# Optimization experiments

Hardware: AMD Instinct MI355X
Metric: run time of the kernel (lower is better)

The kernel has to match this reference:

```python
import jax, jax.numpy as jnp
import numpy as np

C_Z = 128
C_H = 128
L = 512
EPS = 1e-5


def _layer_norm(x, w, b):
    mu = jnp.mean(x, axis=-1, keepdims=True)
    var = jnp.mean(jnp.square(x - mu), axis=-1, keepdims=True)
    return (x - mu) * jax.lax.rsqrt(var + EPS) * w + b


def setup_inputs() -> dict:
    key = jax.random.key(0)
    ks = jax.random.split(key, 10)
    s_z = 1.0 / np.sqrt(C_Z)
    s_h = 1.0 / np.sqrt(C_H)
    return {
        "z": jax.random.normal(ks[0], (L, L, C_Z), dtype=jnp.float32),
        "pair_mask": jax.random.randint(ks[1], (L, L), 0, 2, dtype=jnp.int32),
        "ln_in_w": jnp.ones((C_Z,), jnp.float32),
        "ln_in_b": jnp.zeros((C_Z,), jnp.float32),
        "ln_out_w": jnp.ones((C_H,), jnp.float32),
        "ln_out_b": jnp.zeros((C_H,), jnp.float32),
        # weights stored [in, out] so forward is x @ W
        "W_proj_a": jax.random.uniform(ks[2], (C_Z, C_H), jnp.float32, -s_z, s_z),
        "W_gate_a": jax.random.uniform(ks[3], (C_Z, C_H), jnp.float32, -s_z, s_z),
        "W_proj_b": jax.random.uniform(ks[4], (C_Z, C_H), jnp.float32, -s_z, s_z),
        "W_gate_b": jax.random.uniform(ks[5], (C_Z, C_H), jnp.float32, -s_z, s_z),
        "W_gate_out": jax.random.uniform(ks[6], (C_Z, C_Z), jnp.float32, -s_z, s_z),
        "W_proj_out": jax.random.uniform(ks[7], (C_H, C_Z), jnp.float32, -s_h, s_h),
    }


def reference(z, pair_mask, ln_in_w, ln_in_b, ln_out_w, ln_out_b,
              W_proj_a, W_gate_a, W_proj_b, W_gate_b, W_gate_out, W_proj_out):
    mask = pair_mask.astype(z.dtype)[..., None]  # [L, L, 1]
    z_ln = _layer_norm(z, ln_in_w, ln_in_b)      # [L, L, c_z]
    a = jax.nn.sigmoid(z_ln @ W_gate_a) * (z_ln @ W_proj_a) * mask  # [L, L, c_h]
    b = jax.nn.sigmoid(z_ln @ W_gate_b) * (z_ln @ W_proj_b) * mask  # [L, L, c_h]
    m = jnp.einsum('ikc,jkc->ijc', a, b)         # channel-batched matmul
    m_ln = _layer_norm(m, ln_out_w, ln_out_b)
    g = jax.nn.sigmoid(z_ln @ W_gate_out)        # [L, L, c_z]
    dz = g * (m_ln @ W_proj_out)
    return dz * mask
```

## Files before the change

### kernel.cpp

```cpp
#include <hip/hip_runtime.h>
#include <stdint.h>

#define LDIM 512
#define LLTOT 262144
#define EPSV 1e-5f

typedef short bf16x8 __attribute__((ext_vector_type(8)));
typedef float f32x4 __attribute__((ext_vector_type(4)));

__device__ __forceinline__ unsigned short f2bf(float f) {
  union { float f; unsigned u; } v; v.f = f;
  unsigned r = v.u + 0x7FFFu + ((v.u >> 16) & 1u);
  return (unsigned short)(r >> 16);
}
__device__ __forceinline__ float bf2f(unsigned short h) {
  union { unsigned u; float f; } v; v.u = ((unsigned)h) << 16;
  return v.f;
}
__device__ __forceinline__ float sigm(float x) { return 1.0f / (1.0f + __expf(-x)); }


__global__ void k_prep(const float* __restrict__ Wpa, const float* __restrict__ Wga,
                       const float* __restrict__ Wpb, const float* __restrict__ Wgb,
                       const float* __restrict__ Wgo, const float* __restrict__ Wpo,
                       unsigned short* __restrict__ Wt) {
  int t = blockIdx.x * blockDim.x + threadIdx.x;
  int mat = t >> 14;
  int rem = t & 16383;
  int o = rem >> 7;
  int c = rem & 127;
  const float* src;
  switch (mat) {
    case 0: src = Wga; break;
    case 1: src = Wpa; break;
    case 2: src = Wgb; break;
    case 3: src = Wpb; break;
    case 4: src = Wgo; break;
    default: src = Wpo; break;
  }
  Wt[mat * 16384 + o * 128 + c] = f2bf(src[c * 128 + o]);
}

__global__ __launch_bounds__(256) void k_proj(const float* __restrict__ z,
                                              const float* __restrict__ lnw,
                                              const float* __restrict__ lnb,
                                              const unsigned short* __restrict__ Wt,
                                              const int* __restrict__ maskp,
                                              unsigned short* __restrict__ a_f,
                                              unsigned short* __restrict__ b_f,
                                              unsigned short* __restrict__ gout) {
  __shared__ unsigned char zbuf[128 * 272];
  __shared__ float maskf[128];
  const int t = threadIdx.x;
  const int bid = blockIdx.x;
  const long r0 = (long)bid * 128;
  const int w = t >> 6, lane = t & 63;
  const int mn = lane & 15, q4 = lane >> 4;
  const int k0 = (bid & 3) * 128;
  const int i16 = bid >> 6;
  const int irem = (bid >> 2) & 15;

  if (t < 128) maskf[t] = (float)maskp[r0 + t];

  const float lw0 = lnw[2 * lane], lw1 = lnw[2 * lane + 1];
  const float lb0 = lnb[2 * lane], lb1 = lnb[2 * lane + 1];
#pragma unroll 2
  for (int rr = 0; rr < 32; rr += 4) {
    float2 v[4];
#pragma unroll
    for (int i = 0; i < 4; ++i)
      v[i] = ((const float2*)(z + (r0 + w * 32 + rr + i) * 128))[lane];
#pragma unroll
    for (int i = 0; i < 4; ++i) {
      float s = v[i].x + v[i].y, q = v[i].x * v[i].x + v[i].y * v[i].y;
#pragma unroll
      for (int off = 32; off; off >>= 1) { s += __shfl_xor(s, off); q += __shfl_xor(q, off); }
      float mu = s * (1.0f / 128.0f);
      float rs = rsqrtf(q * (1.0f / 128.0f) - mu * mu + EPSV);
      ushort2 o;
      o.x = f2bf((v[i].x - mu) * rs * lw0 + lb0);
      o.y = f2bf((v[i].y - mu) * rs * lw1 + lb1);
      ((ushort2*)&zbuf[(w * 32 + rr + i) * 272])[lane] = o;
    }
  }
  __syncthreads();

#pragma unroll 1
  for (int p = 0; p < 2; ++p) {
    const unsigned short* Wg = Wt + (p * 2) * 16384;
    const unsigned short* Wp = Wt + (p * 2 + 1) * 16384;
    unsigned short* dst = p ? b_f : a_f;
    bf16x8 wg[2][4], wp[2][4];
#pragma unroll
    for (int ntl = 0; ntl < 2; ++ntl)
#pragma unroll
      for (int kk = 0; kk < 4; ++kk) {
        const int o = (w * 2 + ntl) * 16 + mn;
        wg[ntl][kk] = *(const bf16x8*)(Wg + o * 128 + kk * 32 + q4 * 8);
        wp[ntl][kk] = *(const bf16x8*)(Wp + o * 128 + kk * 32 + q4 * 8);
      }
#pragma unroll 1
    for (int rg = 0; rg < 8; ++rg) {
      bf16x8 afr[4];
#pragma unroll
      for (int kk = 0; kk < 4; ++kk)
        afr[kk] = *(const bf16x8*)(&zbuf[(rg * 16 + mn) * 272 + kk * 64 + q4 * 16]);
      f32x4 aG[2] = {{0.f,0.f,0.f,0.f},{0.f,0.f,0.f,0.f}};
      f32x4 aP[2] = {{0.f,0.f,0.f,0.f},{0.f,0.f,0.f,0.f}};
#pragma unroll
      for (int kk = 0; kk < 4; ++kk)
#pragma unroll
        for (int ntl = 0; ntl < 2; ++ntl) {
          aG[ntl] = __builtin_amdgcn_mfma_f32_16x16x32_bf16(afr[kk], wg[ntl][kk], aG[ntl], 0, 0, 0);
          aP[ntl] = __builtin_amdgcn_mfma_f32_16x16x32_bf16(afr[kk], wp[ntl][kk], aP[ntl], 0, 0, 0);
        }
      const int rowb = rg * 16 + q4 * 4;
      const int kpos = k0 + rowb;
      const int kc = kpos >> 5;
      const int cell = (irem * 4 + ((kpos >> 3) & 3)) * 16 + (kpos & 7) * 2;
#pragma unroll
      for (int ntl = 0; ntl < 2; ++ntl) {
        const int c = (w * 2 + ntl) * 16 + mn;
        unsigned short hv[4];
#pragma unroll
        for (int r = 0; r < 4; ++r)
          hv[r] = f2bf(sigm(aG[ntl][r]) * aP[ntl][r] * maskf[rowb + r]);
        uint2 pk;
        pk.x = (unsigned)hv[0] | ((unsigned)hv[1] << 16);
        pk.y = (unsigned)hv[2] | ((unsigned)hv[3] << 16);
        *(uint2*)((char*)dst + (long)c * 524288 + kc * 32768 + i16 * 1024 + cell) = pk;
      }
    }
  }

  {
    const unsigned short* Wgp = Wt + 4 * 16384;
    bf16x8 wg[2][4];
#pragma unroll
    for (int ntl = 0; ntl < 2; ++ntl)
#pragma unroll
      for (int kk = 0; kk < 4; ++kk)
        wg[ntl][kk] = *(const bf16x8*)(Wgp + ((w * 2 + ntl) * 16 + mn) * 128 + kk * 32 + q4 * 8);
#pragma unroll 1
    for (int rg = 0; rg < 8; ++rg) {
      bf16x8 afr[4];
#pragma unroll
      for (int kk = 0; kk < 4; ++kk)
        afr[kk] = *(const bf16x8*)(&zbuf[(rg * 16 + mn) * 272 + kk * 64 + q4 * 16]);
      f32x4 aG[2] = {{0.f,0.f,0.f,0.f},{0.f,0.f,0.f,0.f}};
#pragma unroll
      for (int kk = 0; kk < 4; ++kk)
#pragma unroll
        for (int ntl = 0; ntl < 2; ++ntl)
          aG[ntl] = __builtin_amdgcn_mfma_f32_16x16x32_bf16(afr[kk], wg[ntl][kk], aG[ntl], 0, 0, 0);
      const int rowb = rg * 16 + q4 * 4;
#pragma unroll
      for (int ntl = 0; ntl < 2; ++ntl) {
        const int c = (w * 2 + ntl) * 16 + mn;
#pragma unroll
        for (int r = 0; r < 4; ++r)
          gout[(r0 + rowb + r) * 128 + c] = f2bf(sigm(aG[ntl][r]));
      }
    }
  }
}

__global__ __launch_bounds__(256) void k_einsum(const unsigned short* __restrict__ af_g,
                                                const unsigned short* __restrict__ bf_g,
                                                unsigned short* __restrict__ m_t) {
  __shared__ unsigned char shm[36864];
  const int t = threadIdx.x;
  const int w = t >> 6, lane = t & 63;
  const int bid = blockIdx.x;
  const int xcd = bid & 7;
  const int j = bid >> 3;
  const int ch = xcd * 16 + (j >> 4);
  const int tile = j & 15;
  const int ti = tile >> 2, tj = tile & 3;
  const int wr = w >> 1, wc = w & 1;
  const int mn = lane & 15, q4 = lane >> 4;
  const int loff = (mn * 4 + q4) * 16;
  const char* Af = (const char*)af_g + (long)ch * 524288 + (ti * 8 + wr * 4) * 1024 + loff;
  const char* Bf = (const char*)bf_g + (long)ch * 524288 + (tj * 8 + wc * 4) * 1024 + loff;

  f32x4 acc[4][4];
#pragma unroll
  for (int i = 0; i < 4; ++i)
#pragma unroll
    for (int jj = 0; jj < 4; ++jj) acc[i][jj] = (f32x4){0.f, 0.f, 0.f, 0.f};

  bf16x8 afr[2][4], bfr[2][4];
#define LOADFRAG(buf, k32)                                                    \
  {                                                                           \
    _Pragma("unroll")                                                         \
    for (int mt = 0; mt < 4; ++mt)                                            \
      afr[buf][mt] = *(const bf16x8*)(Af + (k32) * 32768 + mt * 1024);        \
    _Pragma("unroll")                                                         \
    for (int nt = 0; nt < 4; ++nt)                                            \
      bfr[buf][nt] = *(const bf16x8*)(Bf + (k32) * 32768 + nt * 1024);        \
  }
#define MFMABLK(buf)                                                          \
  {                                                                           \
    _Pragma("unroll")                                                         \
    for (int mt = 0; mt < 4; ++mt)                                            \
      _Pragma("unroll")                                                       \
      for (int nt = 0; nt < 4; ++nt)                                          \
        acc[mt][nt] = __builtin_amdgcn_mfma_f32_16x16x32_bf16(                \
            afr[buf][mt], bfr[buf][nt], acc[mt][nt], 0, 0, 0);                \
  }

  LOADFRAG(0, 0)
#pragma unroll 1
  for (int k32 = 0; k32 < 14; k32 += 2) {
    LOADFRAG(1, k32 + 1)
    MFMABLK(0)
    LOADFRAG(0, k32 + 2)
    MFMABLK(1)
  }
  LOADFRAG(1, 15)
  MFMABLK(0)
  MFMABLK(1)
#undef LOADFRAG
#undef MFMABLK

  unsigned char* eb = shm + w * 9216;
#pragma unroll
  for (int mt = 0; mt < 4; ++mt)
#pragma unroll
    for (int nt = 0; nt < 4; ++nt)
#pragma unroll
      for (int r = 0; r < 4; ++r) {
        int rl = mt * 16 + q4 * 4 + r;
        int cl = nt * 16 + mn;
        *(unsigned short*)(&eb[rl * 144 + cl * 2]) = f2bf(acc[mt][nt][r]);
      }
  char* Mg = (char*)m_t + (long)ch * 524288 +
             (long)(ti * 128 + wr * 64) * 1024 + (tj * 128 + wc * 64) * 2;
#pragma unroll
  for (int it = 0; it < 8; ++it) {
    int rl = it * 8 + (lane >> 3), cc = lane & 7;
    *(int4*)(Mg + (long)rl * 1024 + cc * 16) = *(const int4*)(&eb[rl * 144 + cc * 16]);
  }
}

__global__ __launch_bounds__(256) void k_out(const unsigned short* __restrict__ m_t,
                                             const unsigned short* __restrict__ gbuf,
                                             const unsigned short* __restrict__ Wt,
                                             const int* __restrict__ maskp,
                                             const float* __restrict__ lnw,
                                             const float* __restrict__ lnb,
                                             float* __restrict__ out) {
  __shared__ unsigned char mln[64 * 272];
  __shared__ float obuf[64 * 132];
  __shared__ float lw[128], lb[128], mk[64];
  const int t = threadIdx.x;
  const long r0 = (long)blockIdx.x * 64;

#pragma unroll
  for (int it = 0; it < 4; ++it) {
    int chunk = it * 256 + t;
    int c = chunk >> 3, cc = chunk & 7;
    int4 rv = *(const int4*)((const char*)m_t + (long)c * 524288 + r0 * 2 + cc * 16);
    const unsigned short* rp = (const unsigned short*)&rv;
#pragma unroll
    for (int e = 0; e < 8; ++e) {
      int er = (e + cc) & 7;
      *(unsigned short*)(&mln[(cc * 8 + er) * 272 + c * 2]) = rp[er];
    }
  }
  if (t < 128) { lw[t] = lnw[t]; lb[t] = lnb[t]; }
  if (t < 64) mk[t] = (float)maskp[r0 + t];
  __syncthreads();

  {
    int row = t >> 2, part = t & 3;
    float xv[32];
    float s = 0.f, q = 0.f;
#pragma unroll
    for (int jj = 0; jj < 16; ++jj) {
      unsigned u = *(const unsigned*)(&mln[row * 272 + part * 64 + jj * 4]);
      float x0 = bf2f((unsigned short)(u & 0xffff));
      float x1 = bf2f((unsigned short)(u >> 16));
      xv[2 * jj] = x0; xv[2 * jj + 1] = x1;
      s += x0 + x1; q += x0 * x0 + x1 * x1;
    }
    s += __shfl_xor(s, 1); q += __shfl_xor(q, 1);
    s += __shfl_xor(s, 2); q += __shfl_xor(q, 2);
    float mu = s * (1.f / 128.f);
    float var = q * (1.f / 128.f) - mu * mu;
    float rs = rsqrtf(var + EPSV);
#pragma unroll
    for (int jj = 0; jj < 16; ++jj) {
      int c = part * 32 + 2 * jj;
      unsigned short h0 = f2bf((xv[2 * jj] - mu) * rs * lw[c] + lb[c]);
      unsigned short h1 = f2bf((xv[2 * jj + 1] - mu) * rs * lw[c + 1] + lb[c + 1]);
      *(unsigned*)(&mln[row * 272 + c * 2]) = (unsigned)h0 | ((unsigned)h1 << 16);
    }
  }
  __syncthreads();

  const int w = t >> 6, lane = t & 63;
  const int mn = lane & 15, q4 = lane >> 4;
  bf16x8 afr[4];
#pragma unroll
  for (int kk = 0; kk < 4; ++kk)
    afr[kk] = *(const bf16x8*)(&mln[(w * 16 + mn) * 272 + kk * 64 + q4 * 16]);
  const unsigned short* Wp = Wt + 5 * 16384;
#pragma unroll 1
  for (int nt = 0; nt < 8; ++nt) {
    f32x4 acc = {0.f, 0.f, 0.f, 0.f};
#pragma unroll
    for (int kk = 0; kk < 4; ++kk) {
      bf16x8 bfr = *(const bf16x8*)(Wp + (nt * 16 + mn) * 128 + kk * 32 + q4 * 8);
      acc = __builtin_amdgcn_mfma_f32_16x16x32_bf16(afr[kk], bfr, acc, 0, 0, 0);
    }
    const int cl = nt * 16 + mn;
#pragma unroll
    for (int r = 0; r < 4; ++r)
      obuf[(w * 16 + q4 * 4 + r) * 132 + cl] = acc[r];
  }
  __syncthreads();

#pragma unroll
  for (int it = 0; it < 8; ++it) {
    int chunk = it * 256 + t;
    int row = chunk >> 5, cc = chunk & 31;
    float4 v = *(const float4*)(&obuf[row * 132 + cc * 4]);
    uint2 gp = *(const uint2*)((const char*)gbuf + (r0 + row) * 256 + cc * 8);
    float mval = mk[row];
    v.x *= bf2f((unsigned short)(gp.x & 0xffff)) * mval;
    v.y *= bf2f((unsigned short)(gp.x >> 16)) * mval;
    v.z *= bf2f((unsigned short)(gp.y & 0xffff)) * mval;
    v.w *= bf2f((unsigned short)(gp.y >> 16)) * mval;
    *(float4*)(out + (r0 + row) * 128 + cc * 4) = v;
  }
}

extern "C" void kernel_launch(void* const* d_in, const int* in_sizes, int n_in,
                              void* d_out, int out_size, void* d_ws, size_t ws_size,
                              hipStream_t stream) {
  const float* z    = (const float*)d_in[0];
  const int* maskp  = (const int*)d_in[1];
  const float* lniw = (const float*)d_in[2];
  const float* lnib = (const float*)d_in[3];
  const float* lnow = (const float*)d_in[4];
  const float* lnob = (const float*)d_in[5];
  const float* Wpa  = (const float*)d_in[6];
  const float* Wga  = (const float*)d_in[7];
  const float* Wpb  = (const float*)d_in[8];
  const float* Wgb  = (const float*)d_in[9];
  const float* Wgo  = (const float*)d_in[10];
  const float* Wpo  = (const float*)d_in[11];
  float* out = (float*)d_out;

  char* ws = (char*)d_ws;
  unsigned short* a_f = (unsigned short*)(ws);
  unsigned short* b_f = (unsigned short*)(ws + 67108864);
  unsigned short* g   = (unsigned short*)(ws + 134217728);
  unsigned short* m_t = (unsigned short*)(ws + 201326592);
  unsigned short* Wt  = (unsigned short*)(ws + 268435456);

  k_prep<<<384, 256, 0, stream>>>(Wpa, Wga, Wpb, Wgb, Wgo, Wpo, Wt);
  k_proj<<<2048, 256, 0, stream>>>(z, lniw, lnib, Wt, maskp, a_f, b_f, g);
  k_einsum<<<2048, 256, 0, stream>>>(a_f, b_f, m_t);
  k_out<<<4096, 256, 0, stream>>>(m_t, g, Wt, maskp, lnow, lnob, out);
}
```

Measured before the change: 531.7 us.

## Shrink LDS footprints and rebalance tiles across projection, einsum and output kernels

The projection kernel now handles 64 rows per block instead of 128, doubling the grid and halving its LDS, with the a/b layout index math adjusted to match. The einsum epilogue stages its output through LDS in two halves, halving shared memory so more blocks can be resident. The output kernel gathers four channels per thread into packed LDS writes and drops its float staging buffer, writing the gated, masked result straight from the MFMA accumulators. These changes aim for higher occupancy and fewer LDS transactions, at the cost of less coalesced global stores in the output kernel.

```diff
diff --git a/kernel.cpp b/kernel.cpp
--- a/kernel.cpp
+++ b/kernel.cpp
@@ -49,27 +49,27 @@
                                               unsigned short* __restrict__ a_f,
                                               unsigned short* __restrict__ b_f,
                                               unsigned short* __restrict__ gout) {
-  __shared__ unsigned char zbuf[128 * 272];
-  __shared__ float maskf[128];
+  __shared__ unsigned char zbuf[64 * 272];
+  __shared__ float maskf[64];
   const int t = threadIdx.x;
   const int bid = blockIdx.x;
-  const long r0 = (long)bid * 128;
+  const long r0 = (long)bid * 64;
   const int w = t >> 6, lane = t & 63;
   const int mn = lane & 15, q4 = lane >> 4;
-  const int k0 = (bid & 3) * 128;
-  const int i16 = bid >> 6;
-  const int irem = (bid >> 2) & 15;
-
-  if (t < 128) maskf[t] = (float)maskp[r0 + t];
+  const int k0 = (bid & 7) * 64;
+  const int i16 = bid >> 7;
+  const int irem = (bid >> 3) & 15;
+
+  if (t < 64) maskf[t] = (float)maskp[r0 + t];
 
   const float lw0 = lnw[2 * lane], lw1 = lnw[2 * lane + 1];
   const float lb0 = lnb[2 * lane], lb1 = lnb[2 * lane + 1];
-#pragma unroll 2
-  for (int rr = 0; rr < 32; rr += 4) {
+#pragma unroll
+  for (int rr = 0; rr < 16; rr += 4) {
     float2 v[4];
 #pragma unroll
     for (int i = 0; i < 4; ++i)
-      v[i] = ((const float2*)(z + (r0 + w * 32 + rr + i) * 128))[lane];
+      v[i] = ((const float2*)(z + (r0 + w * 16 + rr + i) * 128))[lane];
 #pragma unroll
     for (int i = 0; i < 4; ++i) {
       float s = v[i].x + v[i].y, q = v[i].x * v[i].x + v[i].y * v[i].y;
@@ -80,7 +80,7 @@
       ushort2 o;
       o.x = f2bf((v[i].x - mu) * rs * lw0 + lb0);
       o.y = f2bf((v[i].y - mu) * rs * lw1 + lb1);
-      ((ushort2*)&zbuf[(w * 32 + rr + i) * 272])[lane] = o;
+      ((ushort2*)&zbuf[(w * 16 + rr + i) * 272])[lane] = o;
     }
   }
   __syncthreads();
@@ -100,7 +100,7 @@
         wp[ntl][kk] = *(const bf16x8*)(Wp + o * 128 + kk * 32 + q4 * 8);
       }
 #pragma unroll 1
-    for (int rg = 0; rg < 8; ++rg) {
+    for (int rg = 0; rg < 4; ++rg) {
       bf16x8 afr[4];
 #pragma unroll
       for (int kk = 0; kk < 4; ++kk)
@@ -142,7 +142,7 @@
       for (int kk = 0; kk < 4; ++kk)
         wg[ntl][kk] = *(const bf16x8*)(Wgp + ((w * 2 + ntl) * 16 + mn) * 128 + kk * 32 + q4 * 8);
 #pragma unroll 1
-    for (int rg = 0; rg < 8; ++rg) {
+    for (int rg = 0; rg < 4; ++rg) {
       bf16x8 afr[4];
 #pragma unroll
       for (int kk = 0; kk < 4; ++kk)
@@ -168,7 +168,7 @@
 __global__ __launch_bounds__(256) void k_einsum(const unsigned short* __restrict__ af_g,
                                                 const unsigned short* __restrict__ bf_g,
                                                 unsigned short* __restrict__ m_t) {
-  __shared__ unsigned char shm[36864];
+  __shared__ unsigned char shm[18432];
   const int t = threadIdx.x;
   const int w = t >> 6, lane = t & 63;
   const int bid = blockIdx.x;
@@ -223,23 +223,29 @@
 #undef LOADFRAG
 #undef MFMABLK
 
-  unsigned char* eb = shm + w * 9216;
-#pragma unroll
-  for (int mt = 0; mt < 4; ++mt)
-#pragma unroll
-    for (int nt = 0; nt < 4; ++nt)
-#pragma unroll
-      for (int r = 0; r < 4; ++r) {
-        int rl = mt * 16 + q4 * 4 + r;
-        int cl = nt * 16 + mn;
-        *(unsigned short*)(&eb[rl * 144 + cl * 2]) = f2bf(acc[mt][nt][r]);
-      }
+  unsigned char* eb = shm + w * 4608;
   char* Mg = (char*)m_t + (long)ch * 524288 +
              (long)(ti * 128 + wr * 64) * 1024 + (tj * 128 + wc * 64) * 2;
-#pragma unroll
-  for (int it = 0; it < 8; ++it) {
-    int rl = it * 8 + (lane >> 3), cc = lane & 7;
-    *(int4*)(Mg + (long)rl * 1024 + cc * 16) = *(const int4*)(&eb[rl * 144 + cc * 16]);
+#pragma unroll 1
+  for (int half = 0; half < 2; ++half) {
+#pragma unroll
+    for (int mh = 0; mh < 2; ++mh) {
+      const int mt = half * 2 + mh;
+#pragma unroll
+      for (int nt = 0; nt < 4; ++nt)
+#pragma unroll
+        for (int r = 0; r < 4; ++r) {
+          int rl = mh * 16 + q4 * 4 + r;
+          int cl = nt * 16 + mn;
+          *(unsigned short*)(&eb[rl * 144 + cl * 2]) = f2bf(acc[mt][nt][r]);
+        }
+    }
+#pragma unroll
+    for (int it = 0; it < 4; ++it) {
+      int rl = it * 8 + (lane >> 3), cc = lane & 7;
+      *(int4*)(Mg + (long)(half * 32 + rl) * 1024 + cc * 16) =
+          *(const int4*)(&eb[rl * 144 + cc * 16]);
+    }
   }
 }
 
@@ -251,21 +257,27 @@
                                              const float* __restrict__ lnb,
                                              float* __restrict__ out) {
   __shared__ unsigned char mln[64 * 272];
-  __shared__ float obuf[64 * 132];
   __shared__ float lw[128], lb[128], mk[64];
   const int t = threadIdx.x;
   const long r0 = (long)blockIdx.x * 64;
 
-#pragma unroll
-  for (int it = 0; it < 4; ++it) {
-    int chunk = it * 256 + t;
-    int c = chunk >> 3, cc = chunk & 7;
-    int4 rv = *(const int4*)((const char*)m_t + (long)c * 524288 + r0 * 2 + cc * 16);
-    const unsigned short* rp = (const unsigned short*)&rv;
+  {
+    const int cgroup = t >> 3;
+    const int cc = t & 7;
+    int4 rv[4];
+#pragma unroll
+    for (int ci = 0; ci < 4; ++ci)
+      rv[ci] = *(const int4*)((const char*)m_t + (long)(cgroup * 4 + ci) * 524288 +
+                              r0 * 2 + cc * 16);
 #pragma unroll
     for (int e = 0; e < 8; ++e) {
       int er = (e + cc) & 7;
-      *(unsigned short*)(&mln[(cc * 8 + er) * 272 + c * 2]) = rp[er];
+      uint2 pk;
+      pk.x = (unsigned)((const unsigned short*)&rv[0])[er] |
+             ((unsigned)((const unsigned short*)&rv[1])[er] << 16);
+      pk.y = (unsigned)((const unsigned short*)&rv[2])[er] |
+             ((unsigned)((const unsigned short*)&rv[3])[er] << 16);
+      *(uint2*)(&mln[(cc * 8 + er) * 272 + cgroup * 8]) = pk;
     }
   }
   if (t < 128) { lw[t] = lnw[t]; lb[t] = lnb[t]; }
@@ -316,23 +328,11 @@
     }
     const int cl = nt * 16 + mn;
 #pragma unroll
-    for (int r = 0; r < 4; ++r)
-      obuf[(w * 16 + q4 * 4 + r) * 132 + cl] = acc[r];
-  }
-  __syncthreads();
-
-#pragma unroll
-  for (int it = 0; it < 8; ++it) {
-    int chunk = it * 256 + t;
-    int row = chunk >> 5, cc = chunk & 31;
-    float4 v = *(const float4*)(&obuf[row * 132 + cc * 4]);
-    uint2 gp = *(const uint2*)((const char*)gbuf + (r0 + row) * 256 + cc * 8);
-    float mval = mk[row];
-    v.x *= bf2f((unsigned short)(gp.x & 0xffff)) * mval;
-    v.y *= bf2f((unsigned short)(gp.x >> 16)) * mval;
-    v.z *= bf2f((unsigned short)(gp.y & 0xffff)) * mval;
-    v.w *= bf2f((unsigned short)(gp.y >> 16)) * mval;
-    *(float4*)(out + (r0 + row) * 128 + cc * 4) = v;
+    for (int r = 0; r < 4; ++r) {
+      const int row = w * 16 + q4 * 4 + r;
+      float gv = bf2f(gbuf[(r0 + row) * 128 + cl]);
+      out[(r0 + row) * 128 + cl] = acc[r] * gv * mk[row];
+    }
   }
 }
 
@@ -361,7 +361,7 @@
   unsigned short* Wt  = (unsigned short*)(ws + 268435456);
 
   k_prep<<<384, 256, 0, stream>>>(Wpa, Wga, Wpb, Wgb, Wgo, Wpo, Wt);
-  k_proj<<<2048, 256, 0, stream>>>(z, lniw, lnib, Wt, maskp, a_f, b_f, g);
+  k_proj<<<4096, 256, 0, stream>>>(z, lniw, lnib, Wt, maskp, a_f, b_f, g);
   k_einsum<<<2048, 256, 0, stream>>>(a_f, b_f, m_t);
   k_out<<<4096, 256, 0, stream>>>(m_t, g, Wt, maskp, lnow, lnob, out);
 }
```

Result: slower. 637.8 us (+20.0%).
